# Performance work log

Hardware: AMD Instinct MI355X
Metric: run time of the kernel (lower is better)

The kernel has to match this reference:

```python
import jax, jax.numpy as jnp
import numpy as np

B, P, F_IN, F_OUT = 4, 256, 512, 512
TAU = 0.07
EPS = 1e-05


def setup_inputs() -> dict:
    key = jax.random.key(0)
    k1, k2, k3 = jax.random.split(key, 3)
    inputs = jax.random.normal(k1, (B, P, F_IN), dtype=jnp.float32)
    labels = jax.random.normal(k2, (B, P, F_IN), dtype=jnp.float32)
    # xavier_uniform for fc.weight (out, in)
    limit = float(np.sqrt(6.0 / (F_IN + F_OUT)))
    W = jax.random.uniform(k3, (F_OUT, F_IN), dtype=jnp.float32, minval=-limit, maxval=limit)
    b = jnp.zeros((F_OUT,), dtype=jnp.float32)
    return {"inputs": inputs, "labels": labels, "W": W, "b": b}


def reference(inputs, labels, W, b):
    Bz, Pn, _ = labels.shape
    # pairwise L1 distance between label vectors: (B, P, P)
    d = jnp.sum(jnp.abs(labels[:, None, :, :] - labels[:, :, None, :]), axis=-1)
    idx = (d == 0).astype(jnp.float32)
    dist = idx / jnp.sum(idx, axis=-1, keepdims=True)  # (B, P, P) target distribution
    # fc + L2 normalize (torch F.normalize: divide by max(norm, 1e-12))
    h = jnp.einsum("bpf,of->bpo", inputs, W) + b
    nrm = jnp.sqrt(jnp.sum(h * h, axis=-1, keepdims=True))
    x = h / jnp.maximum(nrm, 1e-12)
    scores = jnp.einsum("bpd,bqd->bpq", x, x) / TAU
    probs = jnp.clip(jax.nn.softmax(scores, axis=-1), EPS, 1.0 - EPS)
    # kl_div(log(probs), dist, reduction='batchmean'): sum(dist*(log(dist)-log(probs))) / (B*P)
    log_probs = jnp.log(probs)
    pointwise = jnp.where(dist > 0, dist * (jnp.log(jnp.where(dist > 0, dist, 1.0)) - log_probs), 0.0)
    loss = jnp.sum(pointwise) / (Bz * Pn)
    return loss
```

## Files before the change

### kernel.cpp

```cpp
#include <hip/hip_runtime.h>


#define INV_TAU (1.0f / 0.07f)
#define EPSC 1e-5f

constexpr int Bz = 4;
constexpr int Pn = 256;
constexpr int Fdim = 512;
constexpr int Mrows = Bz * Pn;
constexpr size_t HP_STRIDE = (size_t)Mrows * Fdim;
constexpr size_t SP_STRIDE = (size_t)Bz * Pn * Pn;

__device__ __forceinline__ float wave_sum(float v) {
  #pragma unroll
  for (int o = 32; o > 0; o >>= 1) v += __shfl_down(v, o, 64);
  return v;
}
__device__ __forceinline__ float wave_max(float v) {
  #pragma unroll
  for (int o = 32; o > 0; o >>= 1) v = fmaxf(v, __shfl_down(v, o, 64));
  return v;
}
__device__ __forceinline__ unsigned long long mix64(unsigned long long z) {
  z ^= z >> 33; z *= 0xff51afd7ed558ccdULL;
  z ^= z >> 33; z *= 0xc4ceb9fe1a85ec53ULL;
  z ^= z >> 33; return z;
}

__global__ __launch_bounds__(512) void fc_sig(const float* __restrict__ A,
                                              const float* __restrict__ W,
                                              const float* __restrict__ labels,
                                              float* __restrict__ hp,
                                              ulonglong2* __restrict__ sig,
                                              float* __restrict__ acc,
                                              unsigned int* __restrict__ done) {
  const int t = threadIdx.x;
  const int bid = blockIdx.x + 16 * (blockIdx.y + 8 * blockIdx.z);
  if (bid == 0 && t == 0) { acc[0] = 0.0f; done[0] = 0u; }

  {
    const int g = t >> 6, lane = t & 63;
    if (g < 4) {
      const int row = bid * 4 + g;
      const uint4* l4 = (const uint4*)(labels + (size_t)row * Fdim);
      unsigned long long h1 = 0, h2 = 0;
      #pragma unroll
      for (int c = lane; c < Fdim / 4; c += 64) {
        uint4 w = l4[c];
        unsigned long long w01 = ((unsigned long long)w.y << 32) | w.x;
        unsigned long long w23 = ((unsigned long long)w.w << 32) | w.z;
        unsigned long long idx = (unsigned long long)c;
        h1 ^= mix64(w01 + idx * 0x9E3779B97F4A7C15ULL + 0x0123456789ABCDEFULL);
        h1 ^= mix64(w23 + idx * 0xC2B2AE3D27D4EB4FULL + 1ULL);
        h2 ^= mix64(w01 ^ (idx * 0x165667B19E3779F9ULL + 7ULL));
        h2 ^= mix64(w23 ^ (idx * 0x27D4EB2F165667C5ULL + 13ULL));
      }
      #pragma unroll
      for (int o = 32; o > 0; o >>= 1) {
        h1 ^= __shfl_down(h1, o, 64);
        h2 ^= __shfl_down(h2, o, 64);
      }
      if (lane == 0) { sig[row].x = h1; sig[row].y = h2; }
    }
  }

  const int m0 = blockIdx.x * 64, n0 = blockIdx.y * 64;
  const int kbase = blockIdx.z * 256;
  float* C = hp + (size_t)blockIdx.z * HP_STRIDE;
  __shared__ float Ash[32][68];
  __shared__ float Bsh[32][68];
  const int tx = t & 15, ty = t >> 4;
  const int r0 = t >> 3, c0 = (t & 7) << 2;
  float acc2[2][4] = {};

  for (int kc = 0; kc < 256; kc += 32) {
    const float* Ap = A + (size_t)(m0 + r0) * Fdim + kbase + kc + c0;
    const float* Wp = W + (size_t)(n0 + r0) * Fdim + kbase + kc + c0;
    float4 a = *(const float4*)Ap;
    float4 b = *(const float4*)Wp;
    __syncthreads();
    Ash[c0+0][r0] = a.x; Ash[c0+1][r0] = a.y; Ash[c0+2][r0] = a.z; Ash[c0+3][r0] = a.w;
    Bsh[c0+0][r0] = b.x; Bsh[c0+1][r0] = b.y; Bsh[c0+2][r0] = b.z; Bsh[c0+3][r0] = b.w;
    __syncthreads();
    #pragma unroll 8
    for (int k = 0; k < 32; ++k) {
      float2 av = *(const float2*)&Ash[k][ty << 1];
      float4 bv = *(const float4*)&Bsh[k][tx << 2];
      acc2[0][0] = fmaf(av.x, bv.x, acc2[0][0]); acc2[0][1] = fmaf(av.x, bv.y, acc2[0][1]);
      acc2[0][2] = fmaf(av.x, bv.z, acc2[0][2]); acc2[0][3] = fmaf(av.x, bv.w, acc2[0][3]);
      acc2[1][0] = fmaf(av.y, bv.x, acc2[1][0]); acc2[1][1] = fmaf(av.y, bv.y, acc2[1][1]);
      acc2[1][2] = fmaf(av.y, bv.z, acc2[1][2]); acc2[1][3] = fmaf(av.y, bv.w, acc2[1][3]);
    }
  }
  #pragma unroll
  for (int i = 0; i < 2; ++i) {
    float4 o; o.x = acc2[i][0]; o.y = acc2[i][1]; o.z = acc2[i][2]; o.w = acc2[i][3];
    *(float4*)(C + (size_t)(m0 + (ty << 1) + i) * Fdim + n0 + (tx << 2)) = o;
  }
}

__global__ __launch_bounds__(512) void score_gemm(const float* __restrict__ hp,
                                                  const float* __restrict__ bias,
                                                  float* __restrict__ Sp) {
  const int b = blockIdx.z >> 2, kz = blockIdx.z & 3;
  const int kbase = kz * 128;
  const int m0 = blockIdx.x * 64, n0 = blockIdx.y * 64;
  const float* h0 = hp;
  const float* h1 = hp + HP_STRIDE;
  float* C = Sp + (size_t)kz * SP_STRIDE + (size_t)b * Pn * Pn;
  const size_t rb = (size_t)b * Pn;
  __shared__ float Ash[32][68];
  __shared__ float Bsh[32][68];
  const int t = threadIdx.x, tx = t & 15, ty = t >> 4;
  const int r0 = t >> 3, c0 = (t & 7) << 2;
  float acc2[2][4] = {};

  for (int kc = 0; kc < 128; kc += 32) {
    const int ko = kbase + kc + c0;
    float4 bi = *(const float4*)(bias + ko);
    size_t aoff = (rb + m0 + r0) * Fdim + ko;
    size_t boff = (rb + n0 + r0) * Fdim + ko;
    float4 al = *(const float4*)(h0 + aoff);
    float4 ah = *(const float4*)(h1 + aoff);
    float4 bl = *(const float4*)(h0 + boff);
    float4 bh = *(const float4*)(h1 + boff);
    float4 a, b;
    a.x = al.x + ah.x + bi.x; a.y = al.y + ah.y + bi.y;
    a.z = al.z + ah.z + bi.z; a.w = al.w + ah.w + bi.w;
    b.x = bl.x + bh.x + bi.x; b.y = bl.y + bh.y + bi.y;
    b.z = bl.z + bh.z + bi.z; b.w = bl.w + bh.w + bi.w;
    __syncthreads();
    Ash[c0+0][r0] = a.x; Ash[c0+1][r0] = a.y; Ash[c0+2][r0] = a.z; Ash[c0+3][r0] = a.w;
    Bsh[c0+0][r0] = b.x; Bsh[c0+1][r0] = b.y; Bsh[c0+2][r0] = b.z; Bsh[c0+3][r0] = b.w;
    __syncthreads();
    #pragma unroll 8
    for (int k = 0; k < 32; ++k) {
      float2 av = *(const float2*)&Ash[k][ty << 1];
      float4 bv = *(const float4*)&Bsh[k][tx << 2];
      acc2[0][0] = fmaf(av.x, bv.x, acc2[0][0]); acc2[0][1] = fmaf(av.x, bv.y, acc2[0][1]);
      acc2[0][2] = fmaf(av.x, bv.z, acc2[0][2]); acc2[0][3] = fmaf(av.x, bv.w, acc2[0][3]);
      acc2[1][0] = fmaf(av.y, bv.x, acc2[1][0]); acc2[1][1] = fmaf(av.y, bv.y, acc2[1][1]);
      acc2[1][2] = fmaf(av.y, bv.z, acc2[1][2]); acc2[1][3] = fmaf(av.y, bv.w, acc2[1][3]);
    }
  }
  #pragma unroll
  for (int i = 0; i < 2; ++i) {
    float4 o; o.x = acc2[i][0]; o.y = acc2[i][1]; o.z = acc2[i][2]; o.w = acc2[i][3];
    *(float4*)(C + (size_t)(m0 + (ty << 1) + i) * Pn + n0 + (tx << 2)) = o;
  }
}

__global__ __launch_bounds__(256) void loss_kernel(const float* __restrict__ Sp,
                                                   const ulonglong2* __restrict__ sig,
                                                   const float* __restrict__ labels,
                                                   float* __restrict__ acc,
                                                   unsigned int* __restrict__ done,
                                                   float* __restrict__ out) {
  const int bx = blockIdx.x;
  const int b = bx >> 6, p0 = (bx & 63) * 4;
  const int q = threadIdx.x;
  __shared__ float invn[256];
  __shared__ float red[12];
  const float* S0 = Sp + (size_t)b * Pn * Pn;
  const float* S1 = S0 + SP_STRIDE;
  const float* S2 = S0 + 2 * SP_STRIDE;
  const float* S3 = S0 + 3 * SP_STRIDE;

  {
    const int d = q * 257;
    float Sqq = S0[d] + S1[d] + S2[d] + S3[d];
    invn[q] = 1.0f / fmaxf(sqrtf(Sqq), 1e-12f);
  }
  const ulonglong2 sq = sig[(b << 8) + q];
  __syncthreads();

  const int w = q >> 6;
  float lane_contrib = 0.0f;

  #pragma unroll
  for (int i = 0; i < 4; ++i) {
    const int p = p0 + i;
    const int ro = p << 8;
    float Spq = S0[ro + q] + S1[ro + q] + S2[ro + q] + S3[ro + q];
    float s = Spq * invn[p] * invn[q] * INV_TAU;

    ulonglong2 sp = sig[(b << 8) + p];
    bool eq;
    if (q == p) eq = true;
    else if (sp.x == sq.x && sp.y == sq.y) {
      bool v = true;
      const float* lp = labels + (size_t)((b << 8) + p) * Fdim;
      const float* lq = labels + (size_t)((b << 8) + q) * Fdim;
      for (int j = 0; j < Fdim; ++j) v = v && (lp[j] == lq[j]);
      eq = v;
    } else eq = false;

    float m = wave_max(s);
    if ((q & 63) == 0) red[w] = m;
    __syncthreads();
    m = fmaxf(fmaxf(red[0], red[1]), fmaxf(red[2], red[3]));

    float e = expf(s - m);
    float zc = wave_sum(e);
    float cc = wave_sum(eq ? 1.0f : 0.0f);
    if ((q & 63) == 0) { red[4 + w] = zc; red[8 + w] = cc; }
    __syncthreads();
    float z = red[4] + red[5] + red[6] + red[7];
    float n = red[8] + red[9] + red[10] + red[11];

    float prob = fminf(fmaxf(e / z, EPSC), 1.0f - EPSC);
    if (eq) lane_contrib += (-logf(n) - logf(prob)) / n;
    __syncthreads();
  }

  float c = wave_sum(lane_contrib);
  if ((q & 63) == 0) red[w] = c;
  __syncthreads();
  if (q == 0) {
    atomicAdd(acc, red[0] + red[1] + red[2] + red[3]);
    __threadfence();
    unsigned int v = atomicAdd(done, 1u);
    if (v == 255u) {
      float tot = atomicAdd(acc, 0.0f);
      out[0] = tot * (1.0f / (float)(Bz * Pn));
    }
  }
}

extern "C" void kernel_launch(void* const* d_in, const int* in_sizes, int n_in,
                              void* d_out, int out_size, void* d_ws, size_t ws_size,
                              hipStream_t stream) {
  const float* inputs = (const float*)d_in[0];
  const float* labels = (const float*)d_in[1];
  const float* W      = (const float*)d_in[2];
  const float* bias   = (const float*)d_in[3];
  float* out = (float*)d_out;

  char* ws = (char*)d_ws;
  float* acc         = (float*)ws;
  unsigned int* done = (unsigned int*)(ws + 4);
  float* hp = (float*)(ws + 256);
  float* Sp = (float*)(ws + 256 + 2 * HP_STRIDE * 4);
  ulonglong2* sig = (ulonglong2*)(ws + 256 + 2 * HP_STRIDE * 4 + 4 * SP_STRIDE * 4);

  fc_sig<<<dim3(16, 8, 2), 512, 0, stream>>>(inputs, W, labels, hp, sig, acc, done);
  score_gemm<<<dim3(4, 4, 16), 512, 0, stream>>>(hp, bias, Sp);
  loss_kernel<<<256, 256, 0, stream>>>(Sp, sig, labels, acc, done, out);
}
```

Measured before the change: 100.5 us.

## Fuse score GEMM into loss kernel and enlarge FC per-thread tile

Drops the separate score GEMM and its split-K partial-score buffers. Each loss block now computes its 4 rows of dot products against all 256 rows of the batch, plus the row norms, directly from the FC partials using wave reductions. The FC kernel moves to 256 threads with a 4x4 register tile per thread, and every block now runs the label-hash work on all four waves. This removes one launch and the Sp round trip through global memory. In exchange, each of the 256 loss blocks rereads the whole per-batch h matrix and does 5 wave reductions per row, which adds shuffle and serial-loop latency.

```diff
diff --git a/kernel.cpp b/kernel.cpp
--- a/kernel.cpp
+++ b/kernel.cpp
@@ -9,7 +9,6 @@
 constexpr int Fdim = 512;
 constexpr int Mrows = Bz * Pn;
 constexpr size_t HP_STRIDE = (size_t)Mrows * Fdim;
-constexpr size_t SP_STRIDE = (size_t)Bz * Pn * Pn;
 
 __device__ __forceinline__ float wave_sum(float v) {
   #pragma unroll
@@ -27,7 +26,7 @@
   z ^= z >> 33; return z;
 }
 
-__global__ __launch_bounds__(512) void fc_sig(const float* __restrict__ A,
+__global__ __launch_bounds__(256) void fc_sig(const float* __restrict__ A,
                                               const float* __restrict__ W,
                                               const float* __restrict__ labels,
                                               float* __restrict__ hp,
@@ -40,28 +39,26 @@
 
   {
     const int g = t >> 6, lane = t & 63;
-    if (g < 4) {
-      const int row = bid * 4 + g;
-      const uint4* l4 = (const uint4*)(labels + (size_t)row * Fdim);
-      unsigned long long h1 = 0, h2 = 0;
-      #pragma unroll
-      for (int c = lane; c < Fdim / 4; c += 64) {
-        uint4 w = l4[c];
-        unsigned long long w01 = ((unsigned long long)w.y << 32) | w.x;
-        unsigned long long w23 = ((unsigned long long)w.w << 32) | w.z;
-        unsigned long long idx = (unsigned long long)c;
-        h1 ^= mix64(w01 + idx * 0x9E3779B97F4A7C15ULL + 0x0123456789ABCDEFULL);
-        h1 ^= mix64(w23 + idx * 0xC2B2AE3D27D4EB4FULL + 1ULL);
-        h2 ^= mix64(w01 ^ (idx * 0x165667B19E3779F9ULL + 7ULL));
-        h2 ^= mix64(w23 ^ (idx * 0x27D4EB2F165667C5ULL + 13ULL));
-      }
-      #pragma unroll
-      for (int o = 32; o > 0; o >>= 1) {
-        h1 ^= __shfl_down(h1, o, 64);
-        h2 ^= __shfl_down(h2, o, 64);
-      }
-      if (lane == 0) { sig[row].x = h1; sig[row].y = h2; }
-    }
+    const int row = bid * 4 + g;
+    const uint4* l4 = (const uint4*)(labels + (size_t)row * Fdim);
+    unsigned long long h1 = 0, h2 = 0;
+    #pragma unroll
+    for (int c = lane; c < Fdim / 4; c += 64) {
+      uint4 w = l4[c];
+      unsigned long long w01 = ((unsigned long long)w.y << 32) | w.x;
+      unsigned long long w23 = ((unsigned long long)w.w << 32) | w.z;
+      unsigned long long idx = (unsigned long long)c;
+      h1 ^= mix64(w01 + idx * 0x9E3779B97F4A7C15ULL + 0x0123456789ABCDEFULL);
+      h1 ^= mix64(w23 + idx * 0xC2B2AE3D27D4EB4FULL + 1ULL);
+      h2 ^= mix64(w01 ^ (idx * 0x165667B19E3779F9ULL + 7ULL));
+      h2 ^= mix64(w23 ^ (idx * 0x27D4EB2F165667C5ULL + 13ULL));
+    }
+    #pragma unroll
+    for (int o = 32; o > 0; o >>= 1) {
+      h1 ^= __shfl_down(h1, o, 64);
+      h2 ^= __shfl_down(h2, o, 64);
+    }
+    if (lane == 0) { sig[row].x = h1; sig[row].y = h2; }
   }
 
   const int m0 = blockIdx.x * 64, n0 = blockIdx.y * 64;
@@ -71,118 +68,123 @@
   __shared__ float Bsh[32][68];
   const int tx = t & 15, ty = t >> 4;
   const int r0 = t >> 3, c0 = (t & 7) << 2;
-  float acc2[2][4] = {};
+  float a4[4][4] = {};
 
   for (int kc = 0; kc < 256; kc += 32) {
     const float* Ap = A + (size_t)(m0 + r0) * Fdim + kbase + kc + c0;
     const float* Wp = W + (size_t)(n0 + r0) * Fdim + kbase + kc + c0;
-    float4 a = *(const float4*)Ap;
-    float4 b = *(const float4*)Wp;
-    __syncthreads();
-    Ash[c0+0][r0] = a.x; Ash[c0+1][r0] = a.y; Ash[c0+2][r0] = a.z; Ash[c0+3][r0] = a.w;
-    Bsh[c0+0][r0] = b.x; Bsh[c0+1][r0] = b.y; Bsh[c0+2][r0] = b.z; Bsh[c0+3][r0] = b.w;
+    float4 a0 = *(const float4*)Ap;
+    float4 a1 = *(const float4*)(Ap + 32 * Fdim);
+    float4 b0 = *(const float4*)Wp;
+    float4 b1 = *(const float4*)(Wp + 32 * Fdim);
+    __syncthreads();
+    Ash[c0+0][r0] = a0.x; Ash[c0+1][r0] = a0.y; Ash[c0+2][r0] = a0.z; Ash[c0+3][r0] = a0.w;
+    Ash[c0+0][r0+32] = a1.x; Ash[c0+1][r0+32] = a1.y; Ash[c0+2][r0+32] = a1.z; Ash[c0+3][r0+32] = a1.w;
+    Bsh[c0+0][r0] = b0.x; Bsh[c0+1][r0] = b0.y; Bsh[c0+2][r0] = b0.z; Bsh[c0+3][r0] = b0.w;
+    Bsh[c0+0][r0+32] = b1.x; Bsh[c0+1][r0+32] = b1.y; Bsh[c0+2][r0+32] = b1.z; Bsh[c0+3][r0+32] = b1.w;
     __syncthreads();
     #pragma unroll 8
     for (int k = 0; k < 32; ++k) {
-      float2 av = *(const float2*)&Ash[k][ty << 1];
+      float4 av = *(const float4*)&Ash[k][ty << 2];
       float4 bv = *(const float4*)&Bsh[k][tx << 2];
-      acc2[0][0] = fmaf(av.x, bv.x, acc2[0][0]); acc2[0][1] = fmaf(av.x, bv.y, acc2[0][1]);
-      acc2[0][2] = fmaf(av.x, bv.z, acc2[0][2]); acc2[0][3] = fmaf(av.x, bv.w, acc2[0][3]);
-      acc2[1][0] = fmaf(av.y, bv.x, acc2[1][0]); acc2[1][1] = fmaf(av.y, bv.y, acc2[1][1]);
-      acc2[1][2] = fmaf(av.y, bv.z, acc2[1][2]); acc2[1][3] = fmaf(av.y, bv.w, acc2[1][3]);
-    }
-  }
-  #pragma unroll
-  for (int i = 0; i < 2; ++i) {
-    float4 o; o.x = acc2[i][0]; o.y = acc2[i][1]; o.z = acc2[i][2]; o.w = acc2[i][3];
-    *(float4*)(C + (size_t)(m0 + (ty << 1) + i) * Fdim + n0 + (tx << 2)) = o;
-  }
-}
-
-__global__ __launch_bounds__(512) void score_gemm(const float* __restrict__ hp,
+      a4[0][0] = fmaf(av.x, bv.x, a4[0][0]); a4[0][1] = fmaf(av.x, bv.y, a4[0][1]);
+      a4[0][2] = fmaf(av.x, bv.z, a4[0][2]); a4[0][3] = fmaf(av.x, bv.w, a4[0][3]);
+      a4[1][0] = fmaf(av.y, bv.x, a4[1][0]); a4[1][1] = fmaf(av.y, bv.y, a4[1][1]);
+      a4[1][2] = fmaf(av.y, bv.z, a4[1][2]); a4[1][3] = fmaf(av.y, bv.w, a4[1][3]);
+      a4[2][0] = fmaf(av.z, bv.x, a4[2][0]); a4[2][1] = fmaf(av.z, bv.y, a4[2][1]);
+      a4[2][2] = fmaf(av.z, bv.z, a4[2][2]); a4[2][3] = fmaf(av.z, bv.w, a4[2][3]);
+      a4[3][0] = fmaf(av.w, bv.x, a4[3][0]); a4[3][1] = fmaf(av.w, bv.y, a4[3][1]);
+      a4[3][2] = fmaf(av.w, bv.z, a4[3][2]); a4[3][3] = fmaf(av.w, bv.w, a4[3][3]);
+    }
+  }
+  #pragma unroll
+  for (int i = 0; i < 4; ++i) {
+    float4 o; o.x = a4[i][0]; o.y = a4[i][1]; o.z = a4[i][2]; o.w = a4[i][3];
+    *(float4*)(C + (size_t)(m0 + (ty << 2) + i) * Fdim + n0 + (tx << 2)) = o;
+  }
+}
+
+__global__ __launch_bounds__(256) void score_loss(const float* __restrict__ hp,
                                                   const float* __restrict__ bias,
-                                                  float* __restrict__ Sp) {
-  const int b = blockIdx.z >> 2, kz = blockIdx.z & 3;
-  const int kbase = kz * 128;
-  const int m0 = blockIdx.x * 64, n0 = blockIdx.y * 64;
+                                                  const ulonglong2* __restrict__ sig,
+                                                  const float* __restrict__ labels,
+                                                  float* __restrict__ acc,
+                                                  unsigned int* __restrict__ done,
+                                                  float* __restrict__ out) {
+  const int bid = blockIdx.x;
+  const int b = bid >> 6, p0 = (bid & 63) * 4;
+  const int t = threadIdx.x;
+  const int w = t >> 6, lane = t & 63;
+  const int c0 = lane << 3;
+
+  __shared__ float dots[4][256];
+  __shared__ float invn[256];
+  __shared__ float red[12];
+
   const float* h0 = hp;
   const float* h1 = hp + HP_STRIDE;
-  float* C = Sp + (size_t)kz * SP_STRIDE + (size_t)b * Pn * Pn;
-  const size_t rb = (size_t)b * Pn;
-  __shared__ float Ash[32][68];
-  __shared__ float Bsh[32][68];
-  const int t = threadIdx.x, tx = t & 15, ty = t >> 4;
-  const int r0 = t >> 3, c0 = (t & 7) << 2;
-  float acc2[2][4] = {};
-
-  for (int kc = 0; kc < 128; kc += 32) {
-    const int ko = kbase + kc + c0;
-    float4 bi = *(const float4*)(bias + ko);
-    size_t aoff = (rb + m0 + r0) * Fdim + ko;
-    size_t boff = (rb + n0 + r0) * Fdim + ko;
-    float4 al = *(const float4*)(h0 + aoff);
-    float4 ah = *(const float4*)(h1 + aoff);
-    float4 bl = *(const float4*)(h0 + boff);
-    float4 bh = *(const float4*)(h1 + boff);
-    float4 a, b;
-    a.x = al.x + ah.x + bi.x; a.y = al.y + ah.y + bi.y;
-    a.z = al.z + ah.z + bi.z; a.w = al.w + ah.w + bi.w;
-    b.x = bl.x + bh.x + bi.x; b.y = bl.y + bh.y + bi.y;
-    b.z = bl.z + bh.z + bi.z; b.w = bl.w + bh.w + bi.w;
-    __syncthreads();
-    Ash[c0+0][r0] = a.x; Ash[c0+1][r0] = a.y; Ash[c0+2][r0] = a.z; Ash[c0+3][r0] = a.w;
-    Bsh[c0+0][r0] = b.x; Bsh[c0+1][r0] = b.y; Bsh[c0+2][r0] = b.z; Bsh[c0+3][r0] = b.w;
-    __syncthreads();
-    #pragma unroll 8
-    for (int k = 0; k < 32; ++k) {
-      float2 av = *(const float2*)&Ash[k][ty << 1];
-      float4 bv = *(const float4*)&Bsh[k][tx << 2];
-      acc2[0][0] = fmaf(av.x, bv.x, acc2[0][0]); acc2[0][1] = fmaf(av.x, bv.y, acc2[0][1]);
-      acc2[0][2] = fmaf(av.x, bv.z, acc2[0][2]); acc2[0][3] = fmaf(av.x, bv.w, acc2[0][3]);
-      acc2[1][0] = fmaf(av.y, bv.x, acc2[1][0]); acc2[1][1] = fmaf(av.y, bv.y, acc2[1][1]);
-      acc2[1][2] = fmaf(av.y, bv.z, acc2[1][2]); acc2[1][3] = fmaf(av.y, bv.w, acc2[1][3]);
-    }
-  }
-  #pragma unroll
-  for (int i = 0; i < 2; ++i) {
-    float4 o; o.x = acc2[i][0]; o.y = acc2[i][1]; o.z = acc2[i][2]; o.w = acc2[i][3];
-    *(float4*)(C + (size_t)(m0 + (ty << 1) + i) * Pn + n0 + (tx << 2)) = o;
-  }
-}
-
-__global__ __launch_bounds__(256) void loss_kernel(const float* __restrict__ Sp,
-                                                   const ulonglong2* __restrict__ sig,
-                                                   const float* __restrict__ labels,
-                                                   float* __restrict__ acc,
-                                                   unsigned int* __restrict__ done,
-                                                   float* __restrict__ out) {
-  const int bx = blockIdx.x;
-  const int b = bx >> 6, p0 = (bx & 63) * 4;
-  const int q = threadIdx.x;
-  __shared__ float invn[256];
-  __shared__ float red[12];
-  const float* S0 = Sp + (size_t)b * Pn * Pn;
-  const float* S1 = S0 + SP_STRIDE;
-  const float* S2 = S0 + 2 * SP_STRIDE;
-  const float* S3 = S0 + 3 * SP_STRIDE;
+  const float4 bi0 = *(const float4*)(bias + c0);
+  const float4 bi1 = *(const float4*)(bias + c0 + 4);
+
+  float hpr[4][8];
+  #pragma unroll
+  for (int g = 0; g < 4; ++g) {
+    const size_t off = (size_t)((b << 8) + p0 + g) * Fdim + c0;
+    float4 x0 = *(const float4*)(h0 + off);
+    float4 x1 = *(const float4*)(h0 + off + 4);
+    float4 y0 = *(const float4*)(h1 + off);
+    float4 y1 = *(const float4*)(h1 + off + 4);
+    hpr[g][0] = x0.x + y0.x + bi0.x; hpr[g][1] = x0.y + y0.y + bi0.y;
+    hpr[g][2] = x0.z + y0.z + bi0.z; hpr[g][3] = x0.w + y0.w + bi0.w;
+    hpr[g][4] = x1.x + y1.x + bi1.x; hpr[g][5] = x1.y + y1.y + bi1.y;
+    hpr[g][6] = x1.z + y1.z + bi1.z; hpr[g][7] = x1.w + y1.w + bi1.w;
+  }
+
+  for (int i = 0; i < 64; ++i) {
+    const int q = (w << 6) + i;
+    const size_t off = (size_t)((b << 8) + q) * Fdim + c0;
+    float4 x0 = *(const float4*)(h0 + off);
+    float4 x1 = *(const float4*)(h0 + off + 4);
+    float4 y0 = *(const float4*)(h1 + off);
+    float4 y1 = *(const float4*)(h1 + off + 4);
+    float e[8];
+    e[0] = x0.x + y0.x + bi0.x; e[1] = x0.y + y0.y + bi0.y;
+    e[2] = x0.z + y0.z + bi0.z; e[3] = x0.w + y0.w + bi0.w;
+    e[4] = x1.x + y1.x + bi1.x; e[5] = x1.y + y1.y + bi1.y;
+    e[6] = x1.z + y1.z + bi1.z; e[7] = x1.w + y1.w + bi1.w;
+
+    float n2 = 0.f, d0 = 0.f, d1 = 0.f, d2 = 0.f, d3 = 0.f;
+    #pragma unroll
+    for (int j = 0; j < 8; ++j) {
+      n2 = fmaf(e[j], e[j], n2);
+      d0 = fmaf(e[j], hpr[0][j], d0);
+      d1 = fmaf(e[j], hpr[1][j], d1);
+      d2 = fmaf(e[j], hpr[2][j], d2);
+      d3 = fmaf(e[j], hpr[3][j], d3);
+    }
+    n2 = wave_sum(n2);
+    d0 = wave_sum(d0); d1 = wave_sum(d1);
+    d2 = wave_sum(d2); d3 = wave_sum(d3);
+    if (lane == 0) {
+      invn[q] = n2;
+      dots[0][q] = d0; dots[1][q] = d1; dots[2][q] = d2; dots[3][q] = d3;
+    }
+  }
+  __syncthreads();
 
   {
-    const int d = q * 257;
-    float Sqq = S0[d] + S1[d] + S2[d] + S3[d];
-    invn[q] = 1.0f / fmaxf(sqrtf(Sqq), 1e-12f);
-  }
-  const ulonglong2 sq = sig[(b << 8) + q];
+    float n2 = invn[t];
+    invn[t] = 1.0f / fmaxf(sqrtf(n2), 1e-12f);
+  }
+  const ulonglong2 sq = sig[(b << 8) + t];
   __syncthreads();
 
-  const int w = q >> 6;
+  const int q = t;
   float lane_contrib = 0.0f;
-
-  #pragma unroll
-  for (int i = 0; i < 4; ++i) {
-    const int p = p0 + i;
-    const int ro = p << 8;
-    float Spq = S0[ro + q] + S1[ro + q] + S2[ro + q] + S3[ro + q];
-    float s = Spq * invn[p] * invn[q] * INV_TAU;
+  #pragma unroll
+  for (int g = 0; g < 4; ++g) {
+    const int p = p0 + g;
+    float s = dots[g][q] * invn[p] * invn[q] * INV_TAU;
 
     ulonglong2 sp = sig[(b << 8) + p];
     bool eq;
@@ -196,14 +198,14 @@
     } else eq = false;
 
     float m = wave_max(s);
-    if ((q & 63) == 0) red[w] = m;
+    if ((q & 63) == 0) red[q >> 6] = m;
     __syncthreads();
     m = fmaxf(fmaxf(red[0], red[1]), fmaxf(red[2], red[3]));
 
     float e = expf(s - m);
     float zc = wave_sum(e);
     float cc = wave_sum(eq ? 1.0f : 0.0f);
-    if ((q & 63) == 0) { red[4 + w] = zc; red[8 + w] = cc; }
+    if ((q & 63) == 0) { red[4 + (q >> 6)] = zc; red[8 + (q >> 6)] = cc; }
     __syncthreads();
     float z = red[4] + red[5] + red[6] + red[7];
     float n = red[8] + red[9] + red[10] + red[11];
@@ -214,9 +216,9 @@
   }
 
   float c = wave_sum(lane_contrib);
-  if ((q & 63) == 0) red[w] = c;
+  if ((t & 63) == 0) red[t >> 6] = c;
   __syncthreads();
-  if (q == 0) {
+  if (t == 0) {
     atomicAdd(acc, red[0] + red[1] + red[2] + red[3]);
     __threadfence();
     unsigned int v = atomicAdd(done, 1u);
@@ -240,10 +242,8 @@
   float* acc         = (float*)ws;
   unsigned int* done = (unsigned int*)(ws + 4);
   float* hp = (float*)(ws + 256);
-  float* Sp = (float*)(ws + 256 + 2 * HP_STRIDE * 4);
-  ulonglong2* sig = (ulonglong2*)(ws + 256 + 2 * HP_STRIDE * 4 + 4 * SP_STRIDE * 4);
-
-  fc_sig<<<dim3(16, 8, 2), 512, 0, stream>>>(inputs, W, labels, hp, sig, acc, done);
-  score_gemm<<<dim3(4, 4, 16), 512, 0, stream>>>(hp, bias, Sp);
-  loss_kernel<<<256, 256, 0, stream>>>(Sp, sig, labels, acc, done, out);
-}
+  ulonglong2* sig = (ulonglong2*)(ws + 256 + 2 * HP_STRIDE * 4);
+
+  fc_sig<<<dim3(16, 8, 2), 256, 0, stream>>>(inputs, W, labels, hp, sig, acc, done);
+  score_loss<<<256, 256, 0, stream>>>(hp, bias, sig, labels, acc, done, out);
+}
```

After: 134.9 us. +34.2%, slower.
